# Kernel tuning notes

Hardware: AMD Instinct MI355X
Metric: run time of the kernel (lower is better)

Reference implementation:

```python
import jax, jax.numpy as jnp
import numpy as np

H_FEAT, W_FEAT, C_FEAT = 96, 96, 64
UP = 4
HQ, WQ = H_FEAT * UP, W_FEAT * UP
HID, DEPTH = 64, 2
MOD_DIM = HID * 2 * DEPTH          # scale + shift per hidden layer -> 256
HYP_IN = C_FEAT * 9 + 2            # unfolded feat + rel_cell -> 578
HYP_HID = 256


def make_coord(h, w):
    # pixel-center coords in [-1,1], order (y, x) matching (h, w)
    y = ((jnp.arange(h, dtype=jnp.float32) + 0.5) / h) * 2.0 - 1.0
    x = ((jnp.arange(w, dtype=jnp.float32) + 0.5) / w) * 2.0 - 1.0
    yy, xx = jnp.meshgrid(y, x, indexing='ij')
    return jnp.stack([yy, xx], axis=-1)  # (h, w, 2)


def _unfold3(feat):
    # F.unfold(feat, 3, padding=1).view(B, C*9, h, w): channel-major patch order
    B, C, h, w = feat.shape
    p = jnp.pad(feat, ((0, 0), (0, 0), (1, 1), (1, 1)))
    patches = jnp.stack([p[:, :, dy:dy + h, dx:dx + w]
                         for dy in range(3) for dx in range(3)], axis=2)
    return patches.reshape(B, C * 9, h, w)


def _gather_nearest(img, coord):
    # grid_sample(img, coord.flip(-1), mode='nearest', align_corners=False)
    # img: (B, C, H, W); coord: (B, Q, 2) in (y, x) order, range [-1, 1]
    B, C, H, W = img.shape
    iy = jnp.clip(jnp.round((coord[..., 0] + 1.0) * H / 2.0 - 0.5), 0, H - 1).astype(jnp.int32)
    ix = jnp.clip(jnp.round((coord[..., 1] + 1.0) * W / 2.0 - 0.5), 0, W - 1).astype(jnp.int32)
    idx = (iy * W + ix)[:, None, :]                      # (B, 1, Q)
    out = jnp.take_along_axis(img.reshape(B, C, H * W), idx, axis=2)
    return out.transpose(0, 2, 1)                        # (B, Q, C)


def setup_inputs() -> dict:
    key = jax.random.key(0)
    ks = jax.random.split(key, 6)
    s = 0.02
    feat = jax.random.normal(ks[0], (1, C_FEAT, H_FEAT, W_FEAT), jnp.float32)
    coord = make_coord(HQ, WQ).reshape(1, HQ * WQ, 2)
    cell = jnp.broadcast_to(jnp.array([2.0 / HQ, 2.0 / WQ], jnp.float32),
                            (1, HQ * WQ, 2)).astype(jnp.float32)
    return {
        'feat': feat, 'coord': coord, 'cell': cell,
        'Wh1': jax.random.normal(ks[1], (HYP_IN, HYP_HID), jnp.float32) * s,
        'bh1': jnp.zeros((HYP_HID,), jnp.float32),
        'Wh2': jax.random.normal(ks[2], (HYP_HID, MOD_DIM), jnp.float32) * s,
        'bh2': jnp.zeros((MOD_DIM,), jnp.float32),
        'W0': jax.random.normal(ks[3], (C_FEAT + 4, HID), jnp.float32) * s,
        'b0': jnp.zeros((HID,), jnp.float32),
        'W1': jax.random.normal(ks[4], (HID, HID), jnp.float32) * s,
        'b1': jnp.zeros((HID,), jnp.float32),
        'W2': jax.random.normal(ks[5], (HID, 3), jnp.float32) * s,
        'b2': jnp.zeros((3,), jnp.float32),
    }


def reference(feat, coord, cell, Wh1, bh1, Wh2, bh2, W0, b0, W1, b1, W2, b2):
    B, C, h, w = feat.shape
    hw_scale = jnp.array([h, w], jnp.float32)

    # --- gen_feats: 3x3 unfold for the hypernet input ---
    rich = _unfold3(feat)                                   # (B, 9C, h, w)

    # --- gen_modulations: per-latent-pixel hypernet MLP ---
    hyp_in = rich.transpose(0, 2, 3, 1).reshape(B, h * w, C * 9)
    rel_cell_lr = cell[:, :h * w, :] * hw_scale             # cell_decode
    hyp_in = jnp.concatenate([hyp_in, rel_cell_lr], axis=-1)
    mod = jax.nn.relu(hyp_in @ Wh1 + bh1) @ Wh2 + bh2       # (B, h*w, MOD_DIM)
    mod = mod.reshape(B, h, w, MOD_DIM).transpose(0, 3, 1, 2)

    feat_coord = jnp.broadcast_to(
        make_coord(h, w).transpose(2, 0, 1)[None], (B, 2, h, w))

    # --- query_rgb: local-ensemble gather -> modulated MLP -> area blend ---
    rx, ry = 1.0 / h, 1.0 / w                               # 2/h/2, 2/w/2
    eps = 1e-6
    rel_cell_q = cell * hw_scale                            # (B, Q, 2)
    preds, areas = [], []
    for vx in (-1.0, 1.0):
        for vy in (-1.0, 1.0):
            c_ = coord + jnp.array([vx * rx + eps, vy * ry + eps], jnp.float32)
            c_ = jnp.clip(c_, -1.0 + 1e-6, 1.0 - 1e-6)
            q_feat = _gather_nearest(feat, c_)              # (B, Q, C)
            q_coord = _gather_nearest(feat_coord, c_)       # (B, Q, 2)
            q_mod = _gather_nearest(mod, c_)                # (B, Q, MOD_DIM)
            rel = (coord - q_coord) * hw_scale              # (B, Q, 2)
            x = jnp.concatenate([q_feat, rel, rel_cell_q], axis=-1)
            # imnet: hidden layers modulated by (scale, shift) from hypernet
            x = x @ W0 + b0
            x = jax.nn.relu(x * q_mod[..., 0:HID] + q_mod[..., 2 * HID:3 * HID])
            x = x @ W1 + b1
            x = jax.nn.relu(x * q_mod[..., HID:2 * HID] + q_mod[..., 3 * HID:4 * HID])
            preds.append(x @ W2 + b2)                       # (B, Q, 3)
            areas.append(jnp.abs(rel[..., 0] * rel[..., 1]) + 1e-9)

    # diagonal-swap of ensemble areas (LIIF local ensemble)
    areas[0], areas[3] = areas[3], areas[0]
    areas[1], areas[2] = areas[2], areas[1]
    tot = areas[0] + areas[1] + areas[2] + areas[3]
    out = sum(p * (a / tot)[..., None] for p, a in zip(preds, areas))
    return out  # (B, Q, 3)
```

## Files before the change

### kernel.cpp

```cpp
#include <hip/hip_runtime.h>


#define HW 96
#define NPIX (96*96)
#define CFEAT 64
#define INV192 (1.0f/192.0f)

typedef __attribute__((ext_vector_type(8))) short short8;
typedef __attribute__((ext_vector_type(4))) float f32x4;

__device__ __forceinline__ unsigned pack_bf2(float a, float b) {
    unsigned ua = __builtin_bit_cast(unsigned, a);
    unsigned ub = __builtin_bit_cast(unsigned, b);
    return (ua >> 16) | (ub & 0xffff0000u);
}
__device__ __forceinline__ float bf_hi(float a) {
    return __builtin_bit_cast(float, __builtin_bit_cast(unsigned, a) & 0xffff0000u);
}
__device__ __forceinline__ void split8(const float (&v)[8], short8& hi, short8& lo) {
    union { short8 s; unsigned u[4]; } H, L;
    #pragma unroll
    for (int p = 0; p < 4; ++p) {
        float a = v[2*p], b = v[2*p+1];
        H.u[p] = pack_bf2(a, b);
        L.u[p] = pack_bf2(a - bf_hi(a), b - bf_hi(b));
    }
    hi = H.s; lo = L.s;
}
__device__ __forceinline__ unsigned rne16(float x) {
    unsigned u = __builtin_bit_cast(unsigned, x);
    return (u + 0x7fffu + ((u >> 16) & 1u)) >> 16;
}
__device__ __forceinline__ unsigned pack_bf2_rne(float a, float b) {
    return rne16(a) | (rne16(b) << 16);
}
__device__ __forceinline__ short top16(float a) {
    return (short)(__builtin_bit_cast(unsigned, a) >> 16);
}

__device__ __forceinline__ float dpp_red16(float v) {
    int x;
    x = __builtin_amdgcn_update_dpp(0, __builtin_bit_cast(int, v), 0xB1, 0xF, 0xF, true);
    v += __builtin_bit_cast(float, x);
    x = __builtin_amdgcn_update_dpp(0, __builtin_bit_cast(int, v), 0x4E, 0xF, 0xF, true);
    v += __builtin_bit_cast(float, x);
    x = __builtin_amdgcn_update_dpp(0, __builtin_bit_cast(int, v), 0x141, 0xF, 0xF, true);
    v += __builtin_bit_cast(float, x);
    x = __builtin_amdgcn_update_dpp(0, __builtin_bit_cast(int, v), 0x140, 0xF, 0xF, true);
    v += __builtin_bit_cast(float, x);
    return v;
}

#define AXCALC(CV, SGN, II, RR)                                        \
{                                                                      \
    float e = CV + (SGN)*(1.0f/96.0f) + 1e-6f;                         \
    e = fminf(fmaxf(e, -1.0f + 1e-6f), 1.0f - 1e-6f);                  \
    II = (int)rintf((e + 1.0f) * 48.0f - 0.5f);                        \
    II = min(max(II, 0), 95);                                          \
    RR = (CV - fmaf((float)II, 0.0208333333f, -0.9895833333f)) * 96.0f;\
}

__global__ __launch_bounds__(256) void swizzle_kernel(
    const float* __restrict__ Wh1, const float* __restrict__ Wh2,
    const float* __restrict__ W0, const float* __restrict__ W1,
    short* __restrict__ wsw)
{
    const int gid = blockIdx.x*256 + threadIdx.x;
    if (gid >= 432*64) return;
    const int f    = gid >> 6;
    const int lane = gid & 63;
    const int c    = lane & 15;
    const int kg   = lane >> 4;
    const float* W; int kt, nt, N;
    if (f < 288)      { W = Wh1; kt = f >> 4;        nt = f & 15;        N = 256; }
    else if (f < 416) { W = Wh2; kt = (f-288) >> 4;  nt = (f-288) & 15;  N = 256; }
    else if (f < 424) { W = W0;  kt = (f-416) >> 2;  nt = (f-416) & 3;   N = 64;  }
    else              { W = W1;  kt = (f-424) >> 2;  nt = (f-424) & 3;   N = 64;  }
    union { short8 s; unsigned u[4]; } H;
    #pragma unroll
    for (int p = 0; p < 4; ++p) {
        float a = W[(kt*32 + kg*8 + 2*p    )*N + nt*16 + c];
        float b = W[(kt*32 + kg*8 + 2*p + 1)*N + nt*16 + c];
        H.u[p] = pack_bf2_rne(a, b);
    }
    *(short8*)(wsw + (size_t)f*512 + lane*8) = H.s;
}

__global__ __launch_bounds__(512) void hyper_mfma(
    const float* __restrict__ feat,
    const float* __restrict__ cell,
    const float* __restrict__ Wh1,
    const float* __restrict__ bh1,
    const float* __restrict__ bh2,
    const float* __restrict__ b0,
    const short* __restrict__ wsw,
    float* __restrict__ mod_ws,
    float* __restrict__ f0_ws)
{
    __shared__ short AHI[72*128];
    __shared__ short ALO[72*128];
    __shared__ short HHI[32*128];
    __shared__ short HLO[32*128];

    const int tid = threadIdx.x;
    const int blk = blockIdx.x;
    const int y   = blk / 6;
    const int x0  = (blk % 6) * 16;
    const int qbase = y*HW + x0;

    for (int idx = tid; idx < 9216; idx += 512) {
        const int px = idx & 15;
        const int k  = idx >> 4;
        const int ch = k / 9;
        const int j  = k - 9*ch;
        const int dy = j / 3;
        const int dx = j - 3*dy;
        const int gy = y + dy - 1;
        const int gx = x0 + px + dx - 1;
        float v = 0.0f;
        if (gy >= 0 && gy < HW && gx >= 0 && gx < HW)
            v = feat[ch*NPIX + gy*HW + gx];
        const int dst = (k >> 3)*128 + px*8 + (k & 7);
        AHI[dst] = top16(v);
        ALO[dst] = top16(v - bf_hi(v));
    }
    __syncthreads();

    const int lane = tid & 63;
    const int wid  = tid >> 6;
    const int c    = lane & 15;
    const int kg   = lane >> 4;

    const short* wh1f = wsw;
    const short* wh2f = wsw + (size_t)288*512;
    const short* w0f  = wsw + (size_t)416*512;

    if (wid < 4) {
        f32x4 acc0;
        const float bb = b0[wid*16 + c];
        acc0[0] = bb; acc0[1] = bb; acc0[2] = bb; acc0[3] = bb;
        #pragma unroll
        for (int kt = 0; kt < 2; ++kt) {
            float v[8];
            #pragma unroll
            for (int j = 0; j < 8; ++j)
                v[j] = feat[(kt*32 + kg*8 + j)*NPIX + y*HW + x0 + c];
            short8 Ahi, Alo;
            split8(v, Ahi, Alo);
            const short8 B = *(const short8*)(w0f + (size_t)(kt*4 + wid)*512 + lane*8);
            acc0 = __builtin_amdgcn_mfma_f32_16x16x32_bf16(Ahi, B, acc0, 0, 0, 0);
            acc0 = __builtin_amdgcn_mfma_f32_16x16x32_bf16(Alo, B, acc0, 0, 0, 0);
        }
        #pragma unroll
        for (int i = 0; i < 4; ++i)
            f0_ws[(size_t)(qbase + kg*4 + i)*64 + wid*16 + c] = acc0[i];
    }

    f32x4 acc[2];
    #pragma unroll
    for (int nt = 0; nt < 2; ++nt) {
        const float bb = bh1[wid*32 + nt*16 + c];
        acc[nt][0] = bb; acc[nt][1] = bb; acc[nt][2] = bb; acc[nt][3] = bb;
    }
    #pragma unroll
    for (int kt = 0; kt < 18; ++kt) {
        const int aoff = (kt*4 + kg)*128 + c*8;
        const short8 Ahi = *(const short8*)&AHI[aoff];
        const short8 Alo = *(const short8*)&ALO[aoff];
        #pragma unroll
        for (int nt = 0; nt < 2; ++nt) {
            const short8 B = *(const short8*)(wh1f + (size_t)(kt*16 + wid*2 + nt)*512 + lane*8);
            acc[nt] = __builtin_amdgcn_mfma_f32_16x16x32_bf16(Ahi, B, acc[nt], 0, 0, 0);
            acc[nt] = __builtin_amdgcn_mfma_f32_16x16x32_bf16(Alo, B, acc[nt], 0, 0, 0);
        }
    }
    {
        float rc0v[4], rc1v[4];
        #pragma unroll
        for (int i = 0; i < 4; ++i) {
            const int q = qbase + kg*4 + i;
            const float2 ce = ((const float2*)cell)[q];
            rc0v[i] = ce.x * 96.0f;
            rc1v[i] = ce.y * 96.0f;
        }
        #pragma unroll
        for (int nt = 0; nt < 2; ++nt) {
            const int n = wid*32 + nt*16 + c;
            const float w5 = Wh1[576*256 + n];
            const float w6 = Wh1[577*256 + n];
            #pragma unroll
            for (int i = 0; i < 4; ++i) {
                float hv = acc[nt][i] + rc0v[i]*w5 + rc1v[i]*w6;
                hv = fmaxf(hv, 0.0f);
                const int dst = (n >> 3)*128 + (kg*4 + i)*8 + (n & 7);
                HHI[dst] = top16(hv);
                HLO[dst] = top16(hv - bf_hi(hv));
            }
        }
    }
    __syncthreads();

    f32x4 acc2[2];
    #pragma unroll
    for (int nt = 0; nt < 2; ++nt) {
        const float bb = bh2[wid*32 + nt*16 + c];
        acc2[nt][0] = bb; acc2[nt][1] = bb; acc2[nt][2] = bb; acc2[nt][3] = bb;
    }
    #pragma unroll
    for (int kt = 0; kt < 8; ++kt) {
        const int aoff = (kt*4 + kg)*128 + c*8;
        const short8 Ahi = *(const short8*)&HHI[aoff];
        const short8 Alo = *(const short8*)&HLO[aoff];
        #pragma unroll
        for (int nt = 0; nt < 2; ++nt) {
            const short8 B = *(const short8*)(wh2f + (size_t)(kt*16 + wid*2 + nt)*512 + lane*8);
            acc2[nt] = __builtin_amdgcn_mfma_f32_16x16x32_bf16(Ahi, B, acc2[nt], 0, 0, 0);
            acc2[nt] = __builtin_amdgcn_mfma_f32_16x16x32_bf16(Alo, B, acc2[nt], 0, 0, 0);
        }
    }
    #pragma unroll
    for (int nt = 0; nt < 2; ++nt) {
        #pragma unroll
        for (int i = 0; i < 4; ++i)
            mod_ws[(size_t)(qbase + kg*4 + i)*256 + wid*32 + nt*16 + c] = acc2[nt][i];
    }
}

#define ROWQ 324

#define EPI_CALC(S, QY)                                                     \
    const float cy##S = ((float)(QY) + 0.5f) * INV192 - 1.0f;               \
    int iym##S, iyp##S; float r0m##S, r0p##S;                               \
    AXCALC(cy##S, -1.0f, iym##S, r0m##S)                                    \
    AXCALC(cy##S,  1.0f, iyp##S, r0p##S)                                    \
    const int rym##S = (iym##S - ly0)*4 - lx0;                              \
    const int ryp##S = (iyp##S - ly0)*4 - lx0;                              \
    const int lrA##S[4] = { rym##S + ixm, rym##S + ixp,                     \
                            ryp##S + ixm, ryp##S + ixp };                   \
    const float a0##S = fabsf(r0m##S*r1m) + 1e-9f;                          \
    const float a1##S = fabsf(r0m##S*r1p) + 1e-9f;                          \
    const float a2##S = fabsf(r0p##S*r1m) + 1e-9f;                          \
    const float a3##S = fabsf(r0p##S*r1p) + 1e-9f;                          \
    const float invt##S = 1.0f / (a0##S + a1##S + a2##S + a3##S);           \
    const float wgt##S[4] = { a3##S*invt##S, a2##S*invt##S,                 \
                              a1##S*invt##S, a0##S*invt##S };

#define ALOAD(S)                                                            \
    int iyA##S; float r0A##S;                                               \
    AXCALC(cy##S, vxA, iyA##S, r0A##S)                                      \
    const float* rowp##S = smem + ((iyA##S - ly0)*4 + ixAc) * ROWQ;         \
    float4 ga##S[2], gb##S[2], u0a##S[2], u0b##S[2], u1a##S[2], u1b##S[2];  \
    _Pragma("unroll")                                                       \
    for (int kt = 0; kt < 2; ++kt) {                                        \
        const int kb = kt*32 + kg*8;                                        \
        ga##S[kt]  = *(const float4*)(rowp##S + kb);                        \
        gb##S[kt]  = *(const float4*)(rowp##S + kb + 4);                    \
        u0a##S[kt] = *(const float4*)(rowp##S + 64  + kb);                  \
        u0b##S[kt] = *(const float4*)(rowp##S + 64  + kb + 4);              \
        u1a##S[kt] = *(const float4*)(rowp##S + 128 + kb);                  \
        u1b##S[kt] = *(const float4*)(rowp##S + 128 + kb + 4);              \
    }

#define EPI_LOAD(S)                                                         \
    float4 sc2v##S[4], sh2v##S[4];                                          \
    _Pragma("unroll")                                                       \
    for (int i = 0; i < 4; ++i) {                                           \
        sc2v##S[i] = *(const float4*)(smem + lrA##S[i]*ROWQ + 192 + c*4);   \
        sh2v##S[i] = *(const float4*)(smem + lrA##S[i]*ROWQ + 256 + c*4);   \
    }

#define APACK(S)                                                            \
    short8 Afr##S[2];                                                       \
    _Pragma("unroll")                                                       \
    for (int kt = 0; kt < 2; ++kt) {                                        \
        float g[8]  = {ga##S[kt].x, ga##S[kt].y, ga##S[kt].z, ga##S[kt].w,  \
                       gb##S[kt].x, gb##S[kt].y, gb##S[kt].z, gb##S[kt].w}; \
        float u0[8] = {u0a##S[kt].x, u0a##S[kt].y, u0a##S[kt].z, u0a##S[kt].w, \
                       u0b##S[kt].x, u0b##S[kt].y, u0b##S[kt].z, u0b##S[kt].w}; \
        float u1[8] = {u1a##S[kt].x, u1a##S[kt].y, u1a##S[kt].z, u1a##S[kt].w, \
                       u1b##S[kt].x, u1b##S[kt].y, u1b##S[kt].z, u1b##S[kt].w}; \
        union { short8 s; unsigned u[4]; } P;                               \
        _Pragma("unroll")                                                   \
        for (int p = 0; p < 4; ++p) {                                       \
            float h0 = fmaxf(fmaf(r1A, u1[2*p],   fmaf(r0A##S, u0[2*p],   g[2*p]  )), 0.f); \
            float h1 = fmaxf(fmaf(r1A, u1[2*p+1], fmaf(r0A##S, u0[2*p+1], g[2*p+1])), 0.f); \
            P.u[p] = pack_bf2_rne(h0, h1);                                  \
        }                                                                   \
        Afr##S[kt] = P.s;                                                   \
    }

#define MFMA_C(S)                                                           \
    f32x4 acc##S[4];                                                        \
    _Pragma("unroll")                                                       \
    for (int nt = 0; nt < 4; ++nt) {                                        \
        f32x4 z = {b1c[nt], b1c[nt], b1c[nt], b1c[nt]};                     \
        acc##S[nt] = z;                                                     \
        _Pragma("unroll")                                                   \
        for (int kt = 0; kt < 2; ++kt)                                      \
            acc##S[nt] = __builtin_amdgcn_mfma_f32_16x16x32_bf16(Afr##S[kt], Bh[nt][kt], acc##S[nt], 0, 0, 0); \
    }

#define EPIL(S, QY)                                                         \
    {                                                                       \
        float p0 = 0.f, p1 = 0.f, p2 = 0.f;                                 \
        _Pragma("unroll")                                                   \
        for (int i = 0; i < 4; ++i) {                                       \
            const float wi = wgt##S[i];                                     \
            float s0 = 0.f, s1 = 0.f, s2 = 0.f;                             \
            _Pragma("unroll")                                               \
            for (int nt = 0; nt < 4; ++nt) {                                \
                const float sc2 = (nt==0)?sc2v##S[i].x:(nt==1)?sc2v##S[i].y:(nt==2)?sc2v##S[i].z:sc2v##S[i].w; \
                const float sh2 = (nt==0)?sh2v##S[i].x:(nt==1)?sh2v##S[i].y:(nt==2)?sh2v##S[i].z:sh2v##S[i].w; \
                const float v = fmaxf(fmaf(acc##S[nt][i], sc2, sh2), 0.f);  \
                s0 = fmaf(v, w2r[nt][0], s0);                               \
                s1 = fmaf(v, w2r[nt][1], s1);                               \
                s2 = fmaf(v, w2r[nt][2], s2);                               \
            }                                                               \
            p0 = fmaf(s0, wi, p0);                                          \
            p1 = fmaf(s1, wi, p1);                                          \
            p2 = fmaf(s2, wi, p2);                                          \
        }                                                                   \
        p0 = dpp_red16(p0); p1 = dpp_red16(p1); p2 = dpp_red16(p2);         \
        if (c < 3) {                                                        \
            const int qE = (QY)*384 + Xw + kg;                              \
            const float ov = (c == 0) ? p0 + b2v0 : (c == 1) ? p1 + b2v1 : p2 + b2v2; \
            out[(size_t)qE*3 + c] = ov;                                     \
        }                                                                   \
    }

__global__ __launch_bounds__(256, 2) void query_kernel_v10(
    const float* __restrict__ cell,
    const float* __restrict__ W0,
    const short* __restrict__ wsw,
    const float* __restrict__ b1,
    const float* __restrict__ W2,
    const float* __restrict__ b2,
    const float* __restrict__ mod_ws,
    const float* __restrict__ f0_ws,
    float* __restrict__ out)
{
    __shared__ float smem[24*ROWQ];

    const int tid = threadIdx.x;
    const int bX  = blockIdx.x % 48;
    const int bY  = blockIdx.x / 48;
    const int X0  = bX * 8;
    const int Y0  = bY * 16;
    const int lx0 = bX*2 - 1;
    const int ly0 = bY*4 - 1;

    const float rc0 = cell[0] * 96.0f;
    const float rc1 = cell[1] * 96.0f;

    const float4* w64p = (const float4*)(W0 + 64*64);
    const float4* w65p = (const float4*)(W0 + 65*64);
    const float4* w66p = (const float4*)(W0 + 66*64);
    const float4* w67p = (const float4*)(W0 + 67*64);

    for (int idx = tid; idx < 1536; idx += 256) {
        const int r  = idx >> 6;
        const int o  = idx & 63;
        const int ry = r >> 2;
        const int rx = r & 3;
        const int gy = min(max(ly0 + ry, 0), 95);
        const int gx = min(max(lx0 + rx, 0), 95);
        const int src = gy*96 + gx;
        const float4* modv = (const float4*)(mod_ws + (size_t)src*256);
        if (o < 16) {
            const float4 f0 = ((const float4*)(f0_ws + (size_t)src*64))[o];
            const float4 s1 = modv[o];
            const float4 t1 = modv[32 + o];
            const float4 a  = w66p[o];
            const float4 b  = w67p[o];
            float4 v;
            v.x = fmaf(s1.x, fmaf(rc1, b.x, fmaf(rc0, a.x, f0.x)), t1.x);
            v.y = fmaf(s1.y, fmaf(rc1, b.y, fmaf(rc0, a.y, f0.y)), t1.y);
            v.z = fmaf(s1.z, fmaf(rc1, b.z, fmaf(rc0, a.z, f0.z)), t1.z);
            v.w = fmaf(s1.w, fmaf(rc1, b.w, fmaf(rc0, a.w, f0.w)), t1.w);
            *(float4*)(smem + r*ROWQ + o*4) = v;
        } else if (o < 32) {
            const int oo = o - 16;
            const float4 s1 = modv[oo];
            const float4 w  = w64p[oo];
            float4 v = {s1.x*w.x, s1.y*w.y, s1.z*w.z, s1.w*w.w};
            *(float4*)(smem + r*ROWQ + 64 + oo*4) = v;
        } else if (o < 48) {
            const int oo = o - 32;
            const float4 s1 = modv[oo];
            const float4 w  = w65p[oo];
            float4 v = {s1.x*w.x, s1.y*w.y, s1.z*w.z, s1.w*w.w};
            *(float4*)(smem + r*ROWQ + 128 + oo*4) = v;
        } else {
            const int oo = o - 48;
            const float4 s2 = modv[16 + oo];
            const float4 h2 = modv[48 + oo];
            #pragma unroll
            for (int j = 0; j < 4; ++j) {
                const int col = oo*4 + j;
                const int cc  = col & 15;
                const int nt  = col >> 4;
                const float sv = (j==0)?s2.x:(j==1)?s2.y:(j==2)?s2.z:s2.w;
                const float hv = (j==0)?h2.x:(j==1)?h2.y:(j==2)?h2.z:h2.w;
                smem[r*ROWQ + 192 + cc*4 + nt] = sv;
                smem[r*ROWQ + 256 + cc*4 + nt] = hv;
            }
        }
    }

    const int lane = tid & 63;
    const int wid  = tid >> 6;
    const int c    = lane & 15;
    const int kg   = lane >> 4;

    const short* w1f = wsw + (size_t)424*512;
    short8 Bh[4][2];
    #pragma unroll
    for (int kt = 0; kt < 2; ++kt)
        #pragma unroll
        for (int nt = 0; nt < 4; ++nt)
            Bh[nt][kt] = *(const short8*)(w1f + (size_t)(kt*4 + nt)*512 + lane*8);

    float b1c[4];
    float w2r[4][3];
    #pragma unroll
    for (int nt = 0; nt < 4; ++nt) {
        b1c[nt] = b1[nt*16 + c];
        w2r[nt][0] = W2[(nt*16 + c)*3 + 0];
        w2r[nt][1] = W2[(nt*16 + c)*3 + 1];
        w2r[nt][2] = W2[(nt*16 + c)*3 + 2];
    }
    const float b2v0 = b2[0], b2v1 = b2[1], b2v2 = b2[2];

    __syncthreads();

    const int Xw   = X0 + (wid & 1)*4;
    const int Yw   = Y0 + (wid >> 1)*8;
    const int qxA  = c >> 2;
    const int tapA = c & 3;
    const float vxA = (tapA < 2) ? -1.0f : 1.0f;
    const float vyA = (tapA & 1) ? 1.0f : -1.0f;

    const float cxA = ((float)(Xw + qxA) + 0.5f) * INV192 - 1.0f;
    const float cxE = ((float)(Xw + kg)  + 0.5f) * INV192 - 1.0f;
    int ixA; float r1A;
    AXCALC(cxA, vyA, ixA, r1A)
    const int ixAc = ixA - lx0;
    int ixm, ixp; float r1m, r1p;
    AXCALC(cxE, -1.0f, ixm, r1m)
    AXCALC(cxE,  1.0f, ixp, r1p)

    for (int mm = 0; mm < 4; ++mm) {
        const int qyA_ = Yw + 2*mm;
        const int qyB_ = Yw + 2*mm + 1;

        EPI_CALC(A, qyA_)
        EPI_CALC(B, qyB_)
        ALOAD(A)
        ALOAD(B)
        EPI_LOAD(A)
        EPI_LOAD(B)
        APACK(A)
        APACK(B)
        MFMA_C(A)
        MFMA_C(B)
        EPIL(A, qyA_)
        EPIL(B, qyB_)
    }
}

extern "C" void kernel_launch(void* const* d_in, const int* in_sizes, int n_in,
                              void* d_out, int out_size, void* d_ws, size_t ws_size,
                              hipStream_t stream) {
    const float* feat  = (const float*)d_in[0];
    const float* cell  = (const float*)d_in[2];
    const float* Wh1   = (const float*)d_in[3];
    const float* bh1   = (const float*)d_in[4];
    const float* Wh2   = (const float*)d_in[5];
    const float* bh2   = (const float*)d_in[6];
    const float* W0    = (const float*)d_in[7];
    const float* b0    = (const float*)d_in[8];
    const float* W1    = (const float*)d_in[9];
    const float* b1    = (const float*)d_in[10];
    const float* W2    = (const float*)d_in[11];
    const float* b2    = (const float*)d_in[12];
    float* out = (float*)d_out;

    float* mod_ws = (float*)d_ws;
    float* f0_ws  = (float*)d_ws + 9216*256;
    short* wsw    = (short*)((char*)d_ws + 11796480);

    swizzle_kernel<<<dim3(108), dim3(256), 0, stream>>>(Wh1, Wh2, W0, W1, wsw);
    hyper_mfma<<<dim3(576), dim3(512), 0, stream>>>(
        feat, cell, Wh1, bh1, bh2, b0, wsw, mod_ws, f0_ws);
    query_kernel_v10<<<dim3(1152), dim3(256), 0, stream>>>(
        cell, W0, wsw, b1, W2, b2, mod_ws, f0_ws, out);
}
```

Measured before the change: 74.96 us.

## Drop bf16 hi/lo split in hypernet GEMMs and unroll query loop by four

The hypernet kernel stops splitting activations into bf16 high and low halves. It uses a single round-to-nearest bf16 operand, which halves the MFMA count and the LDS footprint for the two hypernet matmuls. The im2col staging loop is reordered so that consecutive threads walk pixels within a channel and tap, which improves coalescing of the feat reads. The query kernel processes four rows per iteration instead of two to expose more independent work, at the cost of register pressure under the two-blocks-per-SM launch bound. Dropping the low-order correction reduces accuracy of the modulation values.

```diff
diff --git a/kernel.cpp b/kernel.cpp
--- a/kernel.cpp
+++ b/kernel.cpp
@@ -34,8 +34,8 @@
 __device__ __forceinline__ unsigned pack_bf2_rne(float a, float b) {
     return rne16(a) | (rne16(b) << 16);
 }
-__device__ __forceinline__ short top16(float a) {
-    return (short)(__builtin_bit_cast(unsigned, a) >> 16);
+__device__ __forceinline__ short rne16s(float x) {
+    return (short)rne16(x);
 }
 
 __device__ __forceinline__ float dpp_red16(float v) {
@@ -98,9 +98,7 @@
     float* __restrict__ f0_ws)
 {
     __shared__ short AHI[72*128];
-    __shared__ short ALO[72*128];
     __shared__ short HHI[32*128];
-    __shared__ short HLO[32*128];
 
     const int tid = threadIdx.x;
     const int blk = blockIdx.x;
@@ -109,20 +107,19 @@
     const int qbase = y*HW + x0;
 
     for (int idx = tid; idx < 9216; idx += 512) {
-        const int px = idx & 15;
-        const int k  = idx >> 4;
-        const int ch = k / 9;
-        const int j  = k - 9*ch;
-        const int dy = j / 3;
-        const int dx = j - 3*dy;
-        const int gy = y + dy - 1;
-        const int gx = x0 + px + dx - 1;
+        const int j   = idx >> 10;
+        const int rem = idx & 1023;
+        const int ch  = rem >> 4;
+        const int px  = rem & 15;
+        const int dy  = j / 3;
+        const int dx  = j - 3*dy;
+        const int k   = ch*9 + j;
+        const int gy  = y + dy - 1;
+        const int gx  = x0 + px + dx - 1;
         float v = 0.0f;
         if (gy >= 0 && gy < HW && gx >= 0 && gx < HW)
             v = feat[ch*NPIX + gy*HW + gx];
-        const int dst = (k >> 3)*128 + px*8 + (k & 7);
-        AHI[dst] = top16(v);
-        ALO[dst] = top16(v - bf_hi(v));
+        AHI[(k >> 3)*128 + px*8 + (k & 7)] = rne16s(v);
     }
     __syncthreads();
 
@@ -164,14 +161,11 @@
     }
     #pragma unroll
     for (int kt = 0; kt < 18; ++kt) {
-        const int aoff = (kt*4 + kg)*128 + c*8;
-        const short8 Ahi = *(const short8*)&AHI[aoff];
-        const short8 Alo = *(const short8*)&ALO[aoff];
+        const short8 A = *(const short8*)&AHI[(kt*4 + kg)*128 + c*8];
         #pragma unroll
         for (int nt = 0; nt < 2; ++nt) {
             const short8 B = *(const short8*)(wh1f + (size_t)(kt*16 + wid*2 + nt)*512 + lane*8);
-            acc[nt] = __builtin_amdgcn_mfma_f32_16x16x32_bf16(Ahi, B, acc[nt], 0, 0, 0);
-            acc[nt] = __builtin_amdgcn_mfma_f32_16x16x32_bf16(Alo, B, acc[nt], 0, 0, 0);
+            acc[nt] = __builtin_amdgcn_mfma_f32_16x16x32_bf16(A, B, acc[nt], 0, 0, 0);
         }
     }
     {
@@ -192,9 +186,7 @@
             for (int i = 0; i < 4; ++i) {
                 float hv = acc[nt][i] + rc0v[i]*w5 + rc1v[i]*w6;
                 hv = fmaxf(hv, 0.0f);
-                const int dst = (n >> 3)*128 + (kg*4 + i)*8 + (n & 7);
-                HHI[dst] = top16(hv);
-                HLO[dst] = top16(hv - bf_hi(hv));
+                HHI[(n >> 3)*128 + (kg*4 + i)*8 + (n & 7)] = rne16s(hv);
             }
         }
     }
@@ -208,14 +200,11 @@
     }
     #pragma unroll
     for (int kt = 0; kt < 8; ++kt) {
-        const int aoff = (kt*4 + kg)*128 + c*8;
-        const short8 Ahi = *(const short8*)&HHI[aoff];
-        const short8 Alo = *(const short8*)&HLO[aoff];
+        const short8 A = *(const short8*)&HHI[(kt*4 + kg)*128 + c*8];
         #pragma unroll
         for (int nt = 0; nt < 2; ++nt) {
             const short8 B = *(const short8*)(wh2f + (size_t)(kt*16 + wid*2 + nt)*512 + lane*8);
-            acc2[nt] = __builtin_amdgcn_mfma_f32_16x16x32_bf16(Ahi, B, acc2[nt], 0, 0, 0);
-            acc2[nt] = __builtin_amdgcn_mfma_f32_16x16x32_bf16(Alo, B, acc2[nt], 0, 0, 0);
+            acc2[nt] = __builtin_amdgcn_mfma_f32_16x16x32_bf16(A, B, acc2[nt], 0, 0, 0);
         }
     }
     #pragma unroll
@@ -328,7 +317,7 @@
         }                                                                   \
     }
 
-__global__ __launch_bounds__(256, 2) void query_kernel_v10(
+__global__ __launch_bounds__(256, 2) void query_kernel_v11(
     const float* __restrict__ cell,
     const float* __restrict__ W0,
     const short* __restrict__ wsw,
@@ -449,22 +438,36 @@
     AXCALC(cxE, -1.0f, ixm, r1m)
     AXCALC(cxE,  1.0f, ixp, r1p)
 
-    for (int mm = 0; mm < 4; ++mm) {
-        const int qyA_ = Yw + 2*mm;
-        const int qyB_ = Yw + 2*mm + 1;
+    for (int mm = 0; mm < 2; ++mm) {
+        const int qyA_ = Yw + 4*mm + 0;
+        const int qyB_ = Yw + 4*mm + 1;
+        const int qyC_ = Yw + 4*mm + 2;
+        const int qyD_ = Yw + 4*mm + 3;
 
         EPI_CALC(A, qyA_)
         EPI_CALC(B, qyB_)
+        EPI_CALC(C, qyC_)
+        EPI_CALC(D, qyD_)
         ALOAD(A)
         ALOAD(B)
+        ALOAD(C)
+        ALOAD(D)
         EPI_LOAD(A)
         EPI_LOAD(B)
+        EPI_LOAD(C)
+        EPI_LOAD(D)
         APACK(A)
         APACK(B)
+        APACK(C)
+        APACK(D)
         MFMA_C(A)
         MFMA_C(B)
+        MFMA_C(C)
+        MFMA_C(D)
         EPIL(A, qyA_)
         EPIL(B, qyB_)
+        EPIL(C, qyC_)
+        EPIL(D, qyD_)
     }
 }
 
@@ -492,6 +495,6 @@
     swizzle_kernel<<<dim3(108), dim3(256), 0, stream>>>(Wh1, Wh2, W0, W1, wsw);
     hyper_mfma<<<dim3(576), dim3(512), 0, stream>>>(
         feat, cell, Wh1, bh1, bh2, b0, wsw, mod_ws, f0_ws);
-    query_kernel_v10<<<dim3(1152), dim3(256), 0, stream>>>(
+    query_kernel_v11<<<dim3(1152), dim3(256), 0, stream>>>(
         cell, W0, wsw, b1, W2, b2, mod_ws, f0_ws, out);
 }
```

Result: no change. 75.16 us (+0.3%).
